# Optimization experiments

Measured on AMD Instinct MI355X. Metric: run time of the kernel, lower is better.

Reference implementation:

```python
import jax, jax.numpy as jnp
import numpy as np

KS = 7           # kernel spatial size (odd)
OMEGA0 = 10.0    # SIREN frequency
PAD = 3          # conv padding ('same' for ks=7)


def _rel_positions_grid(ks):
    # [2, ks, ks], coords in [-1, 1]
    lin = jnp.linspace(-1.0, 1.0, ks, dtype=jnp.float32)
    yy, xx = jnp.meshgrid(lin, lin, indexing='ij')
    return jnp.stack([yy, xx], axis=0)


def _siren(points, W1, b1, W2, b2, W3, b3):
    # points: [..., 3] -> [..., out_ch*in_ch]
    h = jnp.sin(OMEGA0 * (points @ W1 + b1))
    h = jnp.sin(OMEGA0 * (h @ W2 + b2))
    return h @ W3 + b3


def setup_inputs() -> dict:
    key = jax.random.key(0)
    ks = jax.random.split(key, 8)
    B, Cin, Cout, G, H, W, Hid = 16, 32, 32, 8, 64, 64, 32
    x = jax.random.normal(ks[0], (B, Cin, G, H, W), dtype=jnp.float32)
    # deterministic rotation grid on SO(2): angles in [0, 2pi)
    input_g_elems = (jnp.arange(G, dtype=jnp.float32) * (2.0 * jnp.pi / G))[None, :]
    # SIREN params: 3 -> Hid -> Hid -> Cout*Cin
    W1 = jax.random.uniform(ks[1], (3, Hid), minval=-1.0, maxval=1.0) / 3.0
    b1 = jnp.zeros((Hid,), jnp.float32)
    c = jnp.sqrt(6.0 / Hid) / OMEGA0
    W2 = jax.random.uniform(ks[2], (Hid, Hid), minval=-c, maxval=c)
    b2 = jnp.zeros((Hid,), jnp.float32)
    W3 = jax.random.uniform(ks[3], (Hid, Cout * Cin), minval=-c, maxval=c)
    b3 = jnp.zeros((Cout * Cin,), jnp.float32)
    bias = jnp.zeros((1, Cout), jnp.float32)
    return {"x": x, "input_g_elems": input_g_elems, "W1": W1, "b1": b1,
            "W2": W2, "b2": b2, "W3": W3, "b3": b3, "bias": bias}


def reference(x, input_g_elems, W1, b1, W2, b2, W3, b3, bias):
    B, Cin, Gin, H, Wd = x.shape
    Cout = bias.shape[1]
    two_pi = 2.0 * jnp.pi
    rel_pos = _rel_positions_grid(KS)                        # [2, ks, ks]

    # deterministic / non-partial path: g_elems = input_g_elems
    thetas = input_g_elems[0]                                # [G]
    Gout = thetas.shape[0]

    # acted group coords: inv(g) . h = (h - g) mod 2pi, normalized to [-1, 1)
    acted_g = jnp.mod(thetas[None, :] - thetas[:, None], two_pi) / jnp.pi - 1.0  # [Gout, Gin]

    # rotate Rd rel positions by inv(g) = R(-theta)
    ct, st = jnp.cos(-thetas), jnp.sin(-thetas)
    R = jnp.stack([jnp.stack([ct, -st], -1), jnp.stack([st, ct], -1)], -2)  # [Gout,2,2]
    acted_rel = jnp.einsum('gij,jhw->gihw', R, rel_pos)      # [Gout,2,ks,ks]

    # positions fed to kernel net: [Gout, Gin, ks, ks, 3]
    pos_rd = jnp.broadcast_to(acted_rel[:, :, None], (Gout, 2, Gin, KS, KS))
    pos_g = jnp.broadcast_to(acted_g[:, None, :, None, None], (Gout, 1, Gin, KS, KS))
    coords = jnp.concatenate([pos_rd, pos_g], axis=1)        # [Gout,3,Gin,ks,ks]
    points = jnp.moveaxis(coords, 1, -1)                     # [Gout,Gin,ks,ks,3]

    kernel = _siren(points, W1, b1, W2, b2, W3, b3)          # [Gout,Gin,ks,ks,Cout*Cin]
    kernel = kernel.reshape(Gout, Gin, KS, KS, Cout, Cin)
    kernel = jnp.transpose(kernel, (0, 4, 5, 1, 2, 3))       # [Gout,Cout,Cin,Gin,ks,ks]

    # zero kernel outside unit disk of (rotated) Rd positions
    mask = (jnp.linalg.norm(acted_rel, axis=1) <= 1.0)       # [Gout,ks,ks]
    kernel = kernel * mask[:, None, None, None, :, :]

    weight = kernel.reshape(Gout * Cout, Cin * Gin, KS, KS)
    x2 = x.reshape(B, Cin * Gin, H, Wd)
    out = jax.lax.conv_general_dilated(
        x2, weight, window_strides=(1, 1), padding=[(PAD, PAD), (PAD, PAD)],
        dimension_numbers=('NCHW', 'OIHW', 'NCHW'))          # [B, Gout*Cout, H, W]
    out = out.reshape(B, Gout, Cout, H, Wd).transpose(0, 2, 1, 3, 4)  # [B,Cout,Gout,H,W]
    out = out + bias.reshape(1, Cout, 1, 1, 1)
    return out
```

## Files before the change

### kernel.cpp

```cpp
#include <hip/hip_runtime.h>
#include <math.h>

typedef __bf16 bf16_t;
typedef __bf16 bf16x8 __attribute__((ext_vector_type(8)));
typedef float  f32x4  __attribute__((ext_vector_type(4)));

#define B_    16
#define CIN_  32
#define COUT_ 32
#define G_    8
#define CH_   256
#define H_    64
#define W_    64
#define HID_  32
#define KS_   7
#define PAD_  3
#define WP_   70

#define XP_ELEMS   ((size_t)B_ * WP_ * WP_ * CH_)
#define XP_BYTES   (XP_ELEMS * 2)

#define REPACK_BLOCKS (B_ * (H_ + 6))
#define GENW_BLOCKS   (G_ * G_)
#define CONV_BLOCKS   (B_ * (H_ / 2))

static __device__ __forceinline__ unsigned pack_bf16(float a, float b) {
    union { __bf16 h; unsigned short u; } ua, ub;
    ua.h = (__bf16)a; ub.h = (__bf16)b;
    return (unsigned)ua.u | ((unsigned)ub.u << 16);
}

static __device__ __forceinline__ void dma16(const bf16_t* g, bf16_t* l) {
    __builtin_amdgcn_global_load_lds(
        (const __attribute__((address_space(1))) void*)g,
        (__attribute__((address_space(3))) void*)l, 16, 0, 0);
}

__global__ void prep(const float* __restrict__ x, bf16_t* __restrict__ xp,
                     const float* __restrict__ thetas,
                     const float* __restrict__ W1, const float* __restrict__ b1,
                     const float* __restrict__ W2, const float* __restrict__ b2,
                     const float* __restrict__ W3, const float* __restrict__ b3,
                     bf16_t* __restrict__ w2out) {
    __shared__ float h1s[49][33];
    __shared__ float h2s[49][33];
    __shared__ float masks[49];
    int tid = threadIdx.x;
    if (blockIdx.x < REPACK_BLOCKS) {
        int blk = blockIdx.x;
        int b = blk / (H_ + 6), hy = blk % (H_ + 6);
        const int4 z4 = make_int4(0, 0, 0, 0);
        if (hy >= H_) {
            int idx = hy - H_;
            int y = (idx < 3) ? idx : idx + 64;
            bf16_t* dst = xp + ((size_t)(b * WP_) + y) * WP_ * CH_;
            for (int i = tid; i < WP_ * CH_ / 8; i += 256)
                *reinterpret_cast<int4*>(dst + (size_t)i * 8) = z4;
            return;
        }
        int lane = tid & 63, wv = tid >> 6;
        int r = lane >> 3;
        int t = lane & 7;
        size_t orow = ((size_t)(b * WP_) + (hy + 3)) * WP_ * CH_;
        for (int it = 0; it < 8; ++it) {
            int c0 = wv * 8 + it * 32;
            const float* src = x + ((size_t)(b * CH_ + c0 + r)) * (H_ * W_)
                                 + (size_t)hy * W_ + t * 8;
            float4 f0 = *reinterpret_cast<const float4*>(src);
            float4 f1 = *reinterpret_cast<const float4*>(src + 4);
            int d0 = (int)pack_bf16(f0.x, f0.y);
            int d1 = (int)pack_bf16(f0.z, f0.w);
            int d2 = (int)pack_bf16(f1.x, f1.y);
            int d3 = (int)pack_bf16(f1.z, f1.w);
            int p0, p1, p2, p3;
            p0 = __shfl_xor(d0, 32); p1 = __shfl_xor(d1, 32);
            p2 = __shfl_xor(d2, 32); p3 = __shfl_xor(d3, 32);
            if ((r & 4) == 0) { d2 = p0; d3 = p1; } else { d0 = p2; d1 = p3; }
            p0 = __shfl_xor(d0, 16); p1 = __shfl_xor(d1, 16);
            p2 = __shfl_xor(d2, 16); p3 = __shfl_xor(d3, 16);
            if ((r & 2) == 0) { d1 = p0; d3 = p2; } else { d0 = p1; d2 = p3; }
            p0 = __shfl_xor(d0, 8); p1 = __shfl_xor(d1, 8);
            p2 = __shfl_xor(d2, 8); p3 = __shfl_xor(d3, 8);
            if ((r & 1) == 0) {
                d0 = (d0 & 0xFFFF) | (p0 << 16);
                d1 = (d1 & 0xFFFF) | (p1 << 16);
                d2 = (d2 & 0xFFFF) | (p2 << 16);
                d3 = (d3 & 0xFFFF) | (p3 << 16);
            } else {
                d0 = (d0 & 0xFFFF0000) | ((unsigned)p0 >> 16);
                d1 = (d1 & 0xFFFF0000) | ((unsigned)p1 >> 16);
                d2 = (d2 & 0xFFFF0000) | ((unsigned)p2 >> 16);
                d3 = (d3 & 0xFFFF0000) | ((unsigned)p3 >> 16);
            }
            int xpos = t * 8 + r + 3;
            int c16 = c0 >> 3;
            int pp = c16 ^ (xpos & 7);
            int4 v = make_int4(d0, d1, d2, d3);
            *reinterpret_cast<int4*>(xp + orow + (size_t)xpos * CH_ + pp * 8) = v;
        }
        if (tid < 192) {
            int col = tid >> 5, cg = tid & 31;
            int xx = (col < 3) ? col : col + 64;
            *reinterpret_cast<int4*>(xp + orow + (size_t)xx * CH_ + cg * 8) = z4;
        }
        return;
    }
    int blk = blockIdx.x - REPACK_BLOCKS;
    int gin = blk & 7, gout = blk >> 3;
    const float TWO_PI = 6.283185307179586f;
    const float PI_F   = 3.14159265358979323846f;
    float th_o = thetas[gout], th_i = thetas[gin];
    float d = fmodf(th_i - th_o, TWO_PI);
    if (d < 0.0f) d += TWO_PI;
    float ag = d / PI_F - 1.0f;
    float ct = cosf(-th_o), st = sinf(-th_o);

    if (tid < 196) {
        int p = tid >> 2, q = tid & 3;
        int ky = p / 7, kx = p % 7;
        float yy = (float)(ky - 3) / 3.0f;
        float xx = (float)(kx - 3) / 3.0f;
        float r0 = ct * yy - st * xx;
        float r1 = st * yy + ct * xx;
        if (q == 0)
            masks[p] = (r0 * r0 + r1 * r1 <= 1.00001f) ? 1.0f : 0.0f;
        #pragma unroll
        for (int jo = 0; jo < 8; ++jo) {
            int j = q * 8 + jo;
            float a = r0 * W1[j] + r1 * W1[32 + j] + ag * W1[64 + j] + b1[j];
            h1s[p][j] = __sinf(10.0f * a);
        }
    }
    __syncthreads();
    if (tid < 196) {
        int p = tid >> 2, q = tid & 3;
        #pragma unroll
        for (int jo = 0; jo < 8; ++jo) {
            int j = q * 8 + jo;
            float a = b2[j];
            #pragma unroll
            for (int i = 0; i < HID_; ++i) a += h1s[p][i] * W2[i * HID_ + j];
            h2s[p][j] = __sinf(10.0f * a);
        }
    }
    __syncthreads();
    for (int rep = 0; rep < 4; ++rep) {
        int o = rep * 256 + tid;
        float w3c[HID_];
        #pragma unroll
        for (int i = 0; i < HID_; ++i) w3c[i] = W3[i * 1024 + o];
        float bb = b3[o];
        int cout = o >> 5, cin = o & 31;
        int k = cin * G_ + gin;
        int n = gout * COUT_ + cout;
        int kc = k >> 5, hi = (k >> 3) & 3, jj = k & 7;
        bf16_t* dst = w2out + (((size_t)kc * 4 + hi) * 256 + n) * 8 + jj;
        for (int p = 0; p < 49; ++p) {
            float a = bb;
            #pragma unroll
            for (int i = 0; i < HID_; ++i) a += h2s[p][i] * w3c[i];
            a *= masks[p];
            dst[(size_t)p * (8 * 4 * 256 * 8)] = (bf16_t)a;
        }
    }
}

__launch_bounds__(512, 4)
__global__ void conv_mfma(const bf16_t* __restrict__ xp,
                          const bf16_t* __restrict__ w2,
                          const float* __restrict__ bias,
                          float* __restrict__ out) {
    __shared__ __align__(16) bf16_t lds[2][WP_ * CH_];
    int blk = blockIdx.x;
    int b = blk >> 5, h0 = (blk & 31) << 1;
    int tid = threadIdx.x;
    int wv = tid >> 6, lane = tid & 63;
    int m = wv >> 2, ns = wv & 3;
    int lm = lane & 15, lq = lane >> 4;

    f32x4 acc[4][4];
    #pragma unroll
    for (int i = 0; i < 4; ++i)
        #pragma unroll
        for (int j = 0; j < 4; ++j) {
            f32x4 z = {0.0f, 0.0f, 0.0f, 0.0f};
            acc[i][j] = z;
        }

    const bf16_t* rows = xp + (((size_t)(b * WP_) + h0) * WP_) * CH_;
    for (int c = wv; c < 70; c += 8)
        dma16(rows + (size_t)c * 512 + lane * 8, &lds[0][0] + c * 512);
    __syncthreads();

    for (int ky = 0; ky < KS_; ++ky) {
        const bf16_t* slot = &lds[(m + ky) & 1][0];
        #pragma unroll 1
        for (int kx = 0; kx < KS_; ++kx) {
            int tap = ky * KS_ + kx;
            const bf16_t* wbase = w2 + ((size_t)(tap * 32 + lq) * 256 + (ns * 64 + lm)) * 8;
            #pragma unroll 1
            for (int kc = 0; kc < 8; ++kc) {
                const bf16_t* wp = wbase + (size_t)kc * (4 * 256 * 8);
                bf16x8 bfrag[4];
                #pragma unroll
                for (int nt = 0; nt < 4; ++nt)
                    bfrag[nt] = *reinterpret_cast<const bf16x8*>(wp + nt * (16 * 8));
                bf16x8 afrag[4];
                #pragma unroll
                for (int mt = 0; mt < 4; ++mt) {
                    int xr = mt * 16 + lm + kx;
                    int pp = (kc * 4 + lq) ^ (xr & 7);
                    afrag[mt] = *reinterpret_cast<const bf16x8*>(&slot[xr * CH_ + pp * 8]);
                }
                #pragma unroll
                for (int mt = 0; mt < 4; ++mt)
                    #pragma unroll
                    for (int nt = 0; nt < 4; ++nt)
                        acc[mt][nt] = __builtin_amdgcn_mfma_f32_16x16x32_bf16(
                            afrag[mt], bfrag[nt], acc[mt][nt], 0, 0, 0);
            }
        }
        if (ky < KS_ - 1) {
            __syncthreads();
            bf16_t* dstslot = &lds[ky & 1][0];
            const bf16_t* src = rows + (size_t)(ky + 2) * WP_ * CH_;
            for (int c = wv; c < 35; c += 8)
                dma16(src + (size_t)c * 512 + lane * 8, dstslot + c * 512);
            __syncthreads();
        }
    }

    int h = h0 + m;
    #pragma unroll
    for (int mt = 0; mt < 4; ++mt) {
        int wq = mt * 16 + lq * 4;
        #pragma unroll
        for (int nt = 0; nt < 4; ++nt) {
            int n = ns * 64 + nt * 16 + lm;
            int gout = n >> 5, cout = n & 31;
            float bv = bias[cout];
            f32x4 v = acc[mt][nt];
            v[0] += bv; v[1] += bv; v[2] += bv; v[3] += bv;
            float* po = out + (((size_t)(b * COUT_ + cout) * G_ + gout) * (H_ * W_)
                               + h * W_ + wq);
            *reinterpret_cast<f32x4*>(po) = v;
        }
    }
}

extern "C" void kernel_launch(void* const* d_in, const int* in_sizes, int n_in,
                              void* d_out, int out_size, void* d_ws, size_t ws_size,
                              hipStream_t stream) {
    const float* x      = (const float*)d_in[0];
    const float* thetas = (const float*)d_in[1];
    const float* W1     = (const float*)d_in[2];
    const float* b1     = (const float*)d_in[3];
    const float* W2     = (const float*)d_in[4];
    const float* b2     = (const float*)d_in[5];
    const float* W3     = (const float*)d_in[6];
    const float* b3     = (const float*)d_in[7];
    const float* bias   = (const float*)d_in[8];
    float* out = (float*)d_out;

    bf16_t* xp = (bf16_t*)d_ws;
    bf16_t* w2 = (bf16_t*)((char*)d_ws + XP_BYTES);

    hipLaunchKernelGGL(prep, dim3(REPACK_BLOCKS + GENW_BLOCKS), dim3(256), 0, stream,
                       x, xp, thetas, W1, b1, W2, b2, W3, b3, w2);
    hipLaunchKernelGGL(conv_mfma, dim3(CONV_BLOCKS), dim3(512), 0, stream,
                       xp, w2, bias, out);
}
```

Measured before the change: 500.0 us.

## Halve conv block to 4 waves each covering both rows; use channel-major row layout

The conv block drops from 8 waves to 4, and each wave now computes both output rows (8 M-tiles). This lets every B-fragment weight load feed twice as many MFMAs, halving global weight traffic per output. The padded input row layout changes from XOR-swizzled pixel-major to channel-group-major (c16*70+x), so A-fragment LDS reads are contiguous without swizzle arithmetic. The cost is more accumulator registers per thread (128 floats) and fewer waves per block, which may reduce latency hiding.

```diff
diff --git a/kernel.cpp b/kernel.cpp
--- a/kernel.cpp
+++ b/kernel.cpp
@@ -17,7 +17,8 @@
 #define PAD_  3
 #define WP_   70
 
-#define XP_ELEMS   ((size_t)B_ * WP_ * WP_ * CH_)
+#define ROW_ELEMS  (WP_ * CH_)
+#define XP_ELEMS   ((size_t)B_ * WP_ * ROW_ELEMS)
 #define XP_BYTES   (XP_ELEMS * 2)
 
 #define REPACK_BLOCKS (B_ * (H_ + 6))
@@ -53,15 +54,15 @@
         if (hy >= H_) {
             int idx = hy - H_;
             int y = (idx < 3) ? idx : idx + 64;
-            bf16_t* dst = xp + ((size_t)(b * WP_) + y) * WP_ * CH_;
-            for (int i = tid; i < WP_ * CH_ / 8; i += 256)
+            bf16_t* dst = xp + ((size_t)(b * WP_) + y) * ROW_ELEMS;
+            for (int i = tid; i < ROW_ELEMS / 8; i += 256)
                 *reinterpret_cast<int4*>(dst + (size_t)i * 8) = z4;
             return;
         }
         int lane = tid & 63, wv = tid >> 6;
         int r = lane >> 3;
         int t = lane & 7;
-        size_t orow = ((size_t)(b * WP_) + (hy + 3)) * WP_ * CH_;
+        size_t orow = ((size_t)(b * WP_) + (hy + 3)) * ROW_ELEMS;
         for (int it = 0; it < 8; ++it) {
             int c0 = wv * 8 + it * 32;
             const float* src = x + ((size_t)(b * CH_ + c0 + r)) * (H_ * W_)
@@ -94,14 +95,13 @@
             }
             int xpos = t * 8 + r + 3;
             int c16 = c0 >> 3;
-            int pp = c16 ^ (xpos & 7);
             int4 v = make_int4(d0, d1, d2, d3);
-            *reinterpret_cast<int4*>(xp + orow + (size_t)xpos * CH_ + pp * 8) = v;
+            *reinterpret_cast<int4*>(xp + orow + ((size_t)c16 * WP_ + xpos) * 8) = v;
         }
         if (tid < 192) {
             int col = tid >> 5, cg = tid & 31;
             int xx = (col < 3) ? col : col + 64;
-            *reinterpret_cast<int4*>(xp + orow + (size_t)xx * CH_ + cg * 8) = z4;
+            *reinterpret_cast<int4*>(xp + orow + ((size_t)cg * WP_ + xx) * 8) = z4;
         }
         return;
     }
@@ -165,55 +165,56 @@
     }
 }
 
-__launch_bounds__(512, 4)
+__launch_bounds__(256, 2)
 __global__ void conv_mfma(const bf16_t* __restrict__ xp,
                           const bf16_t* __restrict__ w2,
                           const float* __restrict__ bias,
                           float* __restrict__ out) {
-    __shared__ __align__(16) bf16_t lds[2][WP_ * CH_];
+    __shared__ __align__(16) bf16_t lds[2][ROW_ELEMS];
     int blk = blockIdx.x;
     int b = blk >> 5, h0 = (blk & 31) << 1;
     int tid = threadIdx.x;
-    int wv = tid >> 6, lane = tid & 63;
-    int m = wv >> 2, ns = wv & 3;
+    int ns = tid >> 6, lane = tid & 63;
     int lm = lane & 15, lq = lane >> 4;
 
-    f32x4 acc[4][4];
+    f32x4 acc[8][4];
     #pragma unroll
-    for (int i = 0; i < 4; ++i)
+    for (int i = 0; i < 8; ++i)
         #pragma unroll
         for (int j = 0; j < 4; ++j) {
             f32x4 z = {0.0f, 0.0f, 0.0f, 0.0f};
             acc[i][j] = z;
         }
 
-    const bf16_t* rows = xp + (((size_t)(b * WP_) + h0) * WP_) * CH_;
-    for (int c = wv; c < 70; c += 8)
+    const bf16_t* rows = xp + (((size_t)(b * WP_) + h0)) * ROW_ELEMS;
+    for (int c = ns; c < 70; c += 4)
         dma16(rows + (size_t)c * 512 + lane * 8, &lds[0][0] + c * 512);
     __syncthreads();
 
     for (int ky = 0; ky < KS_; ++ky) {
-        const bf16_t* slot = &lds[(m + ky) & 1][0];
+        const bf16_t* slotA = &lds[ky & 1][0];
+        const bf16_t* slotB = &lds[(ky + 1) & 1][0];
         #pragma unroll 1
         for (int kx = 0; kx < KS_; ++kx) {
             int tap = ky * KS_ + kx;
             const bf16_t* wbase = w2 + ((size_t)(tap * 32 + lq) * 256 + (ns * 64 + lm)) * 8;
-            #pragma unroll 1
+            #pragma unroll 2
             for (int kc = 0; kc < 8; ++kc) {
                 const bf16_t* wp = wbase + (size_t)kc * (4 * 256 * 8);
                 bf16x8 bfrag[4];
                 #pragma unroll
                 for (int nt = 0; nt < 4; ++nt)
                     bfrag[nt] = *reinterpret_cast<const bf16x8*>(wp + nt * (16 * 8));
-                bf16x8 afrag[4];
+                int cb = (kc * 4 + lq) * WP_;
+                bf16x8 afrag[8];
                 #pragma unroll
                 for (int mt = 0; mt < 4; ++mt) {
                     int xr = mt * 16 + lm + kx;
-                    int pp = (kc * 4 + lq) ^ (xr & 7);
-                    afrag[mt] = *reinterpret_cast<const bf16x8*>(&slot[xr * CH_ + pp * 8]);
+                    afrag[mt]     = *reinterpret_cast<const bf16x8*>(&slotA[(cb + xr) * 8]);
+                    afrag[mt + 4] = *reinterpret_cast<const bf16x8*>(&slotB[(cb + xr) * 8]);
                 }
                 #pragma unroll
-                for (int mt = 0; mt < 4; ++mt)
+                for (int mt = 0; mt < 8; ++mt)
                     #pragma unroll
                     for (int nt = 0; nt < 4; ++nt)
                         acc[mt][nt] = __builtin_amdgcn_mfma_f32_16x16x32_bf16(
@@ -223,17 +224,17 @@
         if (ky < KS_ - 1) {
             __syncthreads();
             bf16_t* dstslot = &lds[ky & 1][0];
-            const bf16_t* src = rows + (size_t)(ky + 2) * WP_ * CH_;
-            for (int c = wv; c < 35; c += 8)
+            const bf16_t* src = rows + (size_t)(ky + 2) * ROW_ELEMS;
+            for (int c = ns; c < 35; c += 4)
                 dma16(src + (size_t)c * 512 + lane * 8, dstslot + c * 512);
             __syncthreads();
         }
     }
 
-    int h = h0 + m;
     #pragma unroll
-    for (int mt = 0; mt < 4; ++mt) {
-        int wq = mt * 16 + lq * 4;
+    for (int mt = 0; mt < 8; ++mt) {
+        int h = h0 + (mt >> 2);
+        int wq = (mt & 3) * 16 + lq * 4;
         #pragma unroll
         for (int nt = 0; nt < 4; ++nt) {
             int n = ns * 64 + nt * 16 + lm;
@@ -267,6 +268,6 @@
 
     hipLaunchKernelGGL(prep, dim3(REPACK_BLOCKS + GENW_BLOCKS), dim3(256), 0, stream,
                        x, xp, thetas, W1, b1, W2, b2, W3, b3, w2);
-    hipLaunchKernelGGL(conv_mfma, dim3(CONV_BLOCKS), dim3(512), 0, stream,
+    hipLaunchKernelGGL(conv_mfma, dim3(CONV_BLOCKS), dim3(256), 0, stream,
                        xp, w2, bias, out);
 }
```

New measurement: 474.6 us. 5.1% less time.
